# Optimization experiments

Hardware: AMD Instinct MI355X
Metric: run time of the kernel (lower is better)

## Reference

```python
import jax, jax.numpy as jnp
import numpy as np

VOCAB = 32000
EMBED = 512
UNITS = 64  # LSTM hidden size hardcoded in the source
B, T = 32, 128
T_ENC = 128


def setup_inputs() -> dict:
    key = jax.random.key(0)
    ks = jax.random.split(key, 10)
    decoder_inputs = jax.random.randint(ks[0], (B, T), 0, VOCAB)
    encoder_inputs = jax.random.normal(ks[1], (B, T_ENC, UNITS), jnp.float32)
    h0 = 0.1 * jax.random.normal(ks[2], (B, UNITS), jnp.float32)
    c0 = 0.1 * jax.random.normal(ks[3], (B, UNITS), jnp.float32)
    emb = 0.02 * jax.random.normal(ks[4], (VOCAB, EMBED), jnp.float32)
    Wx = 0.05 * jax.random.normal(ks[5], (EMBED, 4 * UNITS), jnp.float32)
    Wh = 0.05 * jax.random.normal(ks[6], (UNITS, 4 * UNITS), jnp.float32)
    # keras unit_forget_bias=True: forget-gate bias initialized to 1
    b = jnp.zeros((4 * UNITS,), jnp.float32).at[UNITS:2 * UNITS].set(1.0)
    Wd = 0.02 * jax.random.normal(ks[7], (2 * UNITS, VOCAB), jnp.float32)
    bd = jnp.zeros((VOCAB,), jnp.float32)
    return {"encoder_inputs": encoder_inputs, "decoder_inputs": decoder_inputs,
            "h0": h0, "c0": c0, "emb": emb, "Wx": Wx, "Wh": Wh, "b": b,
            "Wd": Wd, "bd": bd}


def reference(encoder_inputs, decoder_inputs, h0, c0, emb, Wx, Wh, b, Wd, bd):
    # Embedding (dropout layers are identity at inference)
    x = emb[decoder_inputs]                      # [B, T, E]
    # Precompute input contribution to all gates for all timesteps
    xz = jnp.einsum('bte,eg->btg', x, Wx) + b    # [B, T, 4U]

    def step(carry, zt):
        h, c = carry
        z = zt + h @ Wh                           # [B, 4U]
        i, f, g, o = jnp.split(z, 4, axis=-1)     # keras gate order i,f,c,o
        i = jax.nn.sigmoid(i)
        f = jax.nn.sigmoid(f)
        o = jax.nn.sigmoid(o)
        c_new = f * c + i * jnp.tanh(g)
        h_new = o * jnp.tanh(c_new)
        return (h_new, c_new), h_new

    (hT, cT), hs = jax.lax.scan(step, (h0, c0), jnp.swapaxes(xz, 0, 1))
    seq = jnp.swapaxes(hs, 0, 1)                  # [B, T, U]

    # key_value = concat(h0, seq[:, :-1])  -> queries for Luong attention
    kv = jnp.concatenate([h0[:, None, :], seq[:, :-1, :]], axis=1)  # [B, T, U]
    # keras Attention([q, v]): scores = q @ v^T, softmax, ctx = attn @ v
    scores = jnp.einsum('btu,bsu->bts', kv, encoder_inputs)         # [B, T, T_enc]
    attn = jax.nn.softmax(scores, axis=-1)
    ctx = jnp.einsum('bts,bsu->btu', attn, encoder_inputs)          # [B, T, U]

    feat = jnp.concatenate([seq, ctx], axis=-1)   # [B, T, 2U]
    out = jax.nn.softmax(jnp.einsum('btu,uv->btv', feat, Wd) + bd, axis=-1)
    return out, hT, cT
```

## Files before the change

### kernel.cpp

```cpp
#include <hip/hip_runtime.h>
#include <hip/hip_bf16.h>
#include <math.h>

#define B_   32
#define T_   128
#define TE_  128
#define U_   64
#define E_   512
#define V_   32000
#define G_   256

typedef __attribute__((ext_vector_type(8))) short  short8x;
typedef __attribute__((ext_vector_type(4))) float  f32x4;
typedef __attribute__((ext_vector_type(4))) unsigned short u16x4;

__device__ inline unsigned short f2bf(float x) {
    union { float f; unsigned int u; } v; v.f = x;
    unsigned int u = v.u;
    u = (u + 0x7FFFu + ((u >> 16) & 1u)) >> 16;
    return (unsigned short)u;
}

__global__ void embed_xz_kernel(const int* __restrict__ dec,
                                const float* __restrict__ emb,
                                const float* __restrict__ Wx,
                                const float* __restrict__ bias,
                                float* __restrict__ xz) {
    __shared__ float xs[16][E_];
    int tid = threadIdx.x;
    int rb = blockIdx.x * 16;
#pragma unroll
    for (int i = 0; i < 8; i++) {
        int idx = tid + i * 256;
        int r = idx >> 7, q = idx & 127;
        ((float4*)xs[r])[q] = ((const float4*)(emb + (size_t)dec[rb + r] * E_))[q];
    }
    __syncthreads();
    float acc[16];
#pragma unroll
    for (int r = 0; r < 16; r++) acc[r] = 0.f;
    for (int e = 0; e < E_; e += 4) {
        float w0 = Wx[(e + 0) * G_ + tid];
        float w1 = Wx[(e + 1) * G_ + tid];
        float w2 = Wx[(e + 2) * G_ + tid];
        float w3 = Wx[(e + 3) * G_ + tid];
#pragma unroll
        for (int r = 0; r < 16; r++) {
            float4 xv = *(const float4*)&xs[r][e];
            acc[r] += xv.x * w0 + xv.y * w1 + xv.z * w2 + xv.w * w3;
        }
    }
    float bv = bias[tid];
#pragma unroll
    for (int r = 0; r < 16; r++)
        xz[(size_t)(rb + r) * G_ + tid] = acc[r] + bv;
}

__global__ void lstm_kernel(const float* __restrict__ xz,
                            const float* __restrict__ h0,
                            const float* __restrict__ c0,
                            const float* __restrict__ Wh,
                            float* __restrict__ feat,
                            float* __restrict__ hT,
                            float* __restrict__ cT) {
    int b = blockIdx.x;
    int g = threadIdx.x;
    float w[U_];
#pragma unroll
    for (int u = 0; u < U_; u++) w[u] = Wh[u * G_ + g];
    __shared__ float h[U_];
    __shared__ float c[U_];
    __shared__ float z[G_];
    if (g < U_) { h[g] = h0[b * U_ + g]; c[g] = c0[b * U_ + g]; }
    __syncthreads();
    const float* xzb = xz + (size_t)b * T_ * G_;
    for (int t = 0; t < T_; t++) {
        float acc = xzb[t * G_ + g];
#pragma unroll
        for (int u4 = 0; u4 < U_ / 4; u4++) {
            float4 hv = *(const float4*)&h[u4 * 4];
            acc += hv.x * w[u4 * 4 + 0] + hv.y * w[u4 * 4 + 1] +
                   hv.z * w[u4 * 4 + 2] + hv.w * w[u4 * 4 + 3];
        }
        z[g] = acc;
        __syncthreads();
        if (g < U_) {
            float iv = 1.f / (1.f + expf(-z[g]));
            float fv = 1.f / (1.f + expf(-z[U_ + g]));
            float gv = tanhf(z[2 * U_ + g]);
            float ov = 1.f / (1.f + expf(-z[3 * U_ + g]));
            float cn = fv * c[g] + iv * gv;
            float hn = ov * tanhf(cn);
            c[g] = cn; h[g] = hn;
            feat[((size_t)b * T_ + t) * 2 * U_ + g] = hn;
        }
        __syncthreads();
    }
    if (g < U_) { hT[b * U_ + g] = h[g]; cT[b * U_ + g] = c[g]; }
}

__global__ void attn_kernel(const float* __restrict__ enc,
                            const float* __restrict__ h0,
                            float* __restrict__ feat) {
    int row = blockIdx.x;
    int b = row >> 7;
    int t = row & (T_ - 1);
    int tid = threadIdx.x;
    __shared__ float kv[U_];
    __shared__ float at[TE_];
    __shared__ float red[TE_];
    if (tid < U_)
        kv[tid] = (t == 0) ? h0[b * U_ + tid] : feat[(size_t)(row - 1) * 2 * U_ + tid];
    __syncthreads();
    const float* encb = enc + (size_t)b * TE_ * U_;
    float s = 0.f;
    const float4* e4 = (const float4*)(encb + tid * U_);
#pragma unroll
    for (int u4 = 0; u4 < U_ / 4; u4++) {
        float4 ev = e4[u4];
        s += ev.x * kv[u4 * 4 + 0] + ev.y * kv[u4 * 4 + 1] +
             ev.z * kv[u4 * 4 + 2] + ev.w * kv[u4 * 4 + 3];
    }
    red[tid] = s;
    __syncthreads();
    for (int off = 64; off > 0; off >>= 1) {
        if (tid < off) red[tid] = fmaxf(red[tid], red[tid + off]);
        __syncthreads();
    }
    float m = red[0];
    __syncthreads();
    float e = expf(s - m);
    at[tid] = e;
    red[tid] = e;
    __syncthreads();
    for (int off = 64; off > 0; off >>= 1) {
        if (tid < off) red[tid] += red[tid + off];
        __syncthreads();
    }
    float inv_sum = 1.f / red[0];
    __syncthreads();
    if (tid < U_) {
        float cacc = 0.f;
#pragma unroll 4
        for (int sx = 0; sx < TE_; sx++)
            cacc += at[sx] * encb[sx * U_ + tid];
        feat[(size_t)row * 2 * U_ + U_ + tid] = cacc * inv_sum;
    }
}

__global__ void feat_to_bf16(const float* __restrict__ feat,
                             unsigned short* __restrict__ fb) {
    int i = blockIdx.x * 256 + threadIdx.x;
    float4 v = ((const float4*)feat)[i];
    u16x4 o;
    o.x = f2bf(v.x); o.y = f2bf(v.y); o.z = f2bf(v.z); o.w = f2bf(v.w);
    *(u16x4*)(fb + (size_t)i * 4) = o;
}

__global__ void wd_transpose(const float* __restrict__ Wd,
                             unsigned short* __restrict__ wdt) {
    __shared__ float t[128][65];
    int tid = threadIdx.x;
    int nb = blockIdx.x * 64;
#pragma unroll
    for (int i = 0; i < 32; i++) {
        int idx = tid + i * 256;
        int k = idx >> 6, n = idx & 63;
        t[k][n] = Wd[(size_t)k * V_ + nb + n];
    }
    __syncthreads();
    int n = tid >> 2, kq = tid & 3;
#pragma unroll
    for (int g = 0; g < 4; g++) {
        short8x s;
#pragma unroll
        for (int j = 0; j < 8; j++)
            s[j] = (short)f2bf(t[kq * 32 + g * 8 + j][n]);
        *(short8x*)(wdt + (size_t)(nb + n) * 128 + kq * 32 + g * 8) = s;
    }
}

__device__ inline void gemm_block_map(int L, int& rowblk, int& colblk) {
    int W = (L & 7) * 200 + (L >> 3);
    colblk = W >> 6;
    rowblk = W & 63;
}

__global__ void gemm_stats(const unsigned short* __restrict__ fb,
                           const unsigned short* __restrict__ wdt,
                           const float* __restrict__ bd,
                           float* __restrict__ partial) {
    int rowblk, cb;
    gemm_block_map(blockIdx.x, rowblk, cb);
    int tid = threadIdx.x;
    int lane = tid & 63, wave = tid >> 6;
    int lrow = lane & 15, quad = lane >> 4;
    int rowbase = rowblk * 64 + wave * 16;
    int col0 = cb * 1280;

    short8x a[4];
    const unsigned short* ap = fb + (size_t)(rowbase + lrow) * 128 + quad * 8;
#pragma unroll
    for (int k = 0; k < 4; k++) a[k] = *(const short8x*)(ap + k * 32);

    float s[4] = {0.f, 0.f, 0.f, 0.f};
    for (int ch = 0; ch < 10; ch++) {
        int cc = col0 + ch * 128;
        f32x4 acc[8];
#pragma unroll
        for (int ct = 0; ct < 8; ct++) acc[ct] = {0.f, 0.f, 0.f, 0.f};
        const unsigned short* bp = wdt + (size_t)(cc + lrow) * 128 + quad * 8;
#pragma unroll
        for (int ct = 0; ct < 8; ct++) {
#pragma unroll
            for (int k = 0; k < 4; k++) {
                short8x b = *(const short8x*)(bp + (size_t)ct * 16 * 128 + k * 32);
                acc[ct] = __builtin_amdgcn_mfma_f32_16x16x32_bf16(a[k], b, acc[ct], 0, 0, 0);
            }
        }
#pragma unroll
        for (int ct = 0; ct < 8; ct++) {
            float bdv = bd[cc + ct * 16 + lrow];
#pragma unroll
            for (int r = 0; r < 4; r++)
                s[r] += __expf(acc[ct][r] + bdv);
        }
    }
#pragma unroll
    for (int r = 0; r < 4; r++) {
        float v = s[r];
        v += __shfl_xor(v, 1);
        v += __shfl_xor(v, 2);
        v += __shfl_xor(v, 4);
        v += __shfl_xor(v, 8);
        if (lrow == 0)
            partial[(size_t)(rowbase + quad * 4 + r) * 25 + cb] = v;
    }
}

__global__ void merge_stats(const float* __restrict__ partial,
                            float* __restrict__ inv_s) {
    int r = blockIdx.x * 256 + threadIdx.x;
    float s = 0.f;
#pragma unroll
    for (int i = 0; i < 25; i++) s += partial[(size_t)r * 25 + i];
    inv_s[r] = 1.f / s;
}

__global__ void gemm_norm(const unsigned short* __restrict__ fb,
                          const unsigned short* __restrict__ wdt,
                          const float* __restrict__ bd,
                          const float* __restrict__ inv_s,
                          float* __restrict__ out) {
    __shared__ float lds[64 * 132];
    int rowblkI, cbI;
    gemm_block_map(blockIdx.x, rowblkI, cbI);
    int tid = threadIdx.x;
    int lane = tid & 63, wave = tid >> 6;
    int lrow = lane & 15, quad = lane >> 4;
    int rowblk = rowblkI * 64;
    int rowbase = rowblk + wave * 16;
    int col0 = cbI * 1280;

    short8x a[4];
    const unsigned short* ap = fb + (size_t)(rowbase + lrow) * 128 + quad * 8;
#pragma unroll
    for (int k = 0; k < 4; k++) a[k] = *(const short8x*)(ap + k * 32);

    float inv[4];
#pragma unroll
    for (int r = 0; r < 4; r++) inv[r] = inv_s[rowbase + quad * 4 + r];

    for (int ch = 0; ch < 10; ch++) {
        int cc = col0 + ch * 128;
        f32x4 acc[8];
#pragma unroll
        for (int ct = 0; ct < 8; ct++) acc[ct] = {0.f, 0.f, 0.f, 0.f};
        const unsigned short* bp = wdt + (size_t)(cc + lrow) * 128 + quad * 8;
#pragma unroll
        for (int ct = 0; ct < 8; ct++) {
#pragma unroll
            for (int k = 0; k < 4; k++) {
                short8x b = *(const short8x*)(bp + (size_t)ct * 16 * 128 + k * 32);
                acc[ct] = __builtin_amdgcn_mfma_f32_16x16x32_bf16(a[k], b, acc[ct], 0, 0, 0);
            }
        }
        __syncthreads();
#pragma unroll
        for (int ct = 0; ct < 8; ct++) {
            float bdv = bd[cc + ct * 16 + lrow];
#pragma unroll
            for (int r = 0; r < 4; r++)
                lds[(wave * 16 + quad * 4 + r) * 132 + ct * 16 + lrow] =
                    __expf(acc[ct][r] + bdv) * inv[r];
        }
        __syncthreads();
#pragma unroll
        for (int i = 0; i < 8; i++) {
            int idx = tid + i * 256;
            int r = idx >> 5, c4 = idx & 31;
            f32x4 v = *(f32x4*)&lds[r * 132 + c4 * 4];
            __builtin_nontemporal_store(v,
                (f32x4*)(out + (size_t)(rowblk + r) * V_ + cc + c4 * 4));
        }
    }
}

extern "C" void kernel_launch(void* const* d_in, const int* in_sizes, int n_in,
                              void* d_out, int out_size, void* d_ws, size_t ws_size,
                              hipStream_t stream) {
    const float* enc  = (const float*)d_in[0];
    const int*   dec  = (const int*)d_in[1];
    const float* h0   = (const float*)d_in[2];
    const float* c0   = (const float*)d_in[3];
    const float* emb  = (const float*)d_in[4];
    const float* Wx   = (const float*)d_in[5];
    const float* Wh   = (const float*)d_in[6];
    const float* bias = (const float*)d_in[7];
    const float* Wd   = (const float*)d_in[8];
    const float* bd   = (const float*)d_in[9];
    float* out = (float*)d_out;
    float* ws  = (float*)d_ws;

    const int NROW = B_ * T_;
    float* xz      = ws;
    float* feat    = xz + (size_t)NROW * G_;
    float* partial = feat + (size_t)NROW * 2 * U_;
    float* inv_s   = partial + (size_t)NROW * 25;
    unsigned short* fb  = (unsigned short*)(inv_s + NROW);
    unsigned short* wdt = (unsigned short*)(fb + (size_t)NROW * 2 * U_);
    float* hT = out + (size_t)NROW * V_;
    float* cT = hT + B_ * U_;

    wd_transpose<<<dim3(V_ / 64), 256, 0, stream>>>(Wd, wdt);
    embed_xz_kernel<<<dim3(NROW / 16), 256, 0, stream>>>(dec, emb, Wx, bias, xz);
    lstm_kernel<<<dim3(B_), 256, 0, stream>>>(xz, h0, c0, Wh, feat, hT, cT);
    attn_kernel<<<dim3(NROW), 128, 0, stream>>>(enc, h0, feat);
    feat_to_bf16<<<dim3(NROW * 2 * U_ / 1024), 256, 0, stream>>>(feat, fb);
    gemm_stats<<<dim3(1600), 256, 0, stream>>>(fb, wdt, bd, partial);
    merge_stats<<<dim3(NROW / 256), 256, 0, stream>>>(partial, inv_s);
    gemm_norm<<<dim3(1600), 256, 0, stream>>>(fb, wdt, bd, inv_s, out);
}
```

Baseline: 1.222 ms.

## Double GEMM row tiles, fuse bf16 conversion, and prefetch xz in LSTM

Each wave in both vocab GEMM kernels now computes two 16-row tiles, so every B fragment loaded from wdt feeds two MFMAs. This halves the grid and the redundant weight traffic. The bf16 conversion kernel is removed: the LSTM and attention kernels write bf16 features directly. The LSTM loop also prefetches the next timestep's xz and splits the dot product into four independent accumulators to shorten the dependency chain. The costs are higher register pressure in the GEMMs and fewer blocks for occupancy.

```diff
diff --git a/kernel.cpp b/kernel.cpp
--- a/kernel.cpp
+++ b/kernel.cpp
@@ -61,6 +61,7 @@
                             const float* __restrict__ c0,
                             const float* __restrict__ Wh,
                             float* __restrict__ feat,
+                            unsigned short* __restrict__ fb,
                             float* __restrict__ hT,
                             float* __restrict__ cT) {
     int b = blockIdx.x;
@@ -72,17 +73,29 @@
     __shared__ float c[U_];
     __shared__ float z[G_];
     if (g < U_) { h[g] = h0[b * U_ + g]; c[g] = c0[b * U_ + g]; }
-    __syncthreads();
     const float* xzb = xz + (size_t)b * T_ * G_;
+    float xznext = xzb[g];
+    __syncthreads();
     for (int t = 0; t < T_; t++) {
-        float acc = xzb[t * G_ + g];
-#pragma unroll
-        for (int u4 = 0; u4 < U_ / 4; u4++) {
-            float4 hv = *(const float4*)&h[u4 * 4];
-            acc += hv.x * w[u4 * 4 + 0] + hv.y * w[u4 * 4 + 1] +
-                   hv.z * w[u4 * 4 + 2] + hv.w * w[u4 * 4 + 3];
-        }
-        z[g] = acc;
+        float ac0 = xznext, ac1 = 0.f, ac2 = 0.f, ac3 = 0.f;
+        int tn = (t + 1 < T_) ? t + 1 : t;
+        xznext = xzb[tn * G_ + g];
+#pragma unroll
+        for (int u4 = 0; u4 < 16; u4 += 4) {
+            float4 h0v = *(const float4*)&h[(u4 + 0) * 4];
+            float4 h1v = *(const float4*)&h[(u4 + 1) * 4];
+            float4 h2v = *(const float4*)&h[(u4 + 2) * 4];
+            float4 h3v = *(const float4*)&h[(u4 + 3) * 4];
+            ac0 += h0v.x * w[(u4+0)*4+0] + h0v.y * w[(u4+0)*4+1] +
+                   h0v.z * w[(u4+0)*4+2] + h0v.w * w[(u4+0)*4+3];
+            ac1 += h1v.x * w[(u4+1)*4+0] + h1v.y * w[(u4+1)*4+1] +
+                   h1v.z * w[(u4+1)*4+2] + h1v.w * w[(u4+1)*4+3];
+            ac2 += h2v.x * w[(u4+2)*4+0] + h2v.y * w[(u4+2)*4+1] +
+                   h2v.z * w[(u4+2)*4+2] + h2v.w * w[(u4+2)*4+3];
+            ac3 += h3v.x * w[(u4+3)*4+0] + h3v.y * w[(u4+3)*4+1] +
+                   h3v.z * w[(u4+3)*4+2] + h3v.w * w[(u4+3)*4+3];
+        }
+        z[g] = (ac0 + ac1) + (ac2 + ac3);
         __syncthreads();
         if (g < U_) {
             float iv = 1.f / (1.f + expf(-z[g]));
@@ -92,7 +105,9 @@
             float cn = fv * c[g] + iv * gv;
             float hn = ov * tanhf(cn);
             c[g] = cn; h[g] = hn;
-            feat[((size_t)b * T_ + t) * 2 * U_ + g] = hn;
+            size_t row = (size_t)b * T_ + t;
+            feat[row * 2 * U_ + g] = hn;
+            fb[row * 2 * U_ + g] = f2bf(hn);
         }
         __syncthreads();
     }
@@ -101,7 +116,8 @@
 
 __global__ void attn_kernel(const float* __restrict__ enc,
                             const float* __restrict__ h0,
-                            float* __restrict__ feat) {
+                            const float* __restrict__ feat,
+                            unsigned short* __restrict__ fb) {
     int row = blockIdx.x;
     int b = row >> 7;
     int t = row & (T_ - 1);
@@ -144,17 +160,8 @@
 #pragma unroll 4
         for (int sx = 0; sx < TE_; sx++)
             cacc += at[sx] * encb[sx * U_ + tid];
-        feat[(size_t)row * 2 * U_ + U_ + tid] = cacc * inv_sum;
-    }
-}
-
-__global__ void feat_to_bf16(const float* __restrict__ feat,
-                             unsigned short* __restrict__ fb) {
-    int i = blockIdx.x * 256 + threadIdx.x;
-    float4 v = ((const float4*)feat)[i];
-    u16x4 o;
-    o.x = f2bf(v.x); o.y = f2bf(v.y); o.z = f2bf(v.z); o.w = f2bf(v.w);
-    *(u16x4*)(fb + (size_t)i * 4) = o;
+        fb[(size_t)row * 2 * U_ + U_ + tid] = f2bf(cacc * inv_sum);
+    }
 }
 
 __global__ void wd_transpose(const float* __restrict__ Wd,
@@ -181,9 +188,9 @@
 }
 
 __device__ inline void gemm_block_map(int L, int& rowblk, int& colblk) {
-    int W = (L & 7) * 200 + (L >> 3);
-    colblk = W >> 6;
-    rowblk = W & 63;
+    int W = (L & 7) * 100 + (L >> 3);
+    colblk = W >> 5;
+    rowblk = W & 31;
 }
 
 __global__ void gemm_stats(const unsigned short* __restrict__ fb,
@@ -195,47 +202,57 @@
     int tid = threadIdx.x;
     int lane = tid & 63, wave = tid >> 6;
     int lrow = lane & 15, quad = lane >> 4;
-    int rowbase = rowblk * 64 + wave * 16;
+    int rowbase = rowblk * 128 + wave * 32;
     int col0 = cb * 1280;
 
-    short8x a[4];
-    const unsigned short* ap = fb + (size_t)(rowbase + lrow) * 128 + quad * 8;
-#pragma unroll
-    for (int k = 0; k < 4; k++) a[k] = *(const short8x*)(ap + k * 32);
-
-    float s[4] = {0.f, 0.f, 0.f, 0.f};
+    short8x a[2][4];
+#pragma unroll
+    for (int rt = 0; rt < 2; rt++) {
+        const unsigned short* ap = fb + (size_t)(rowbase + rt * 16 + lrow) * 128 + quad * 8;
+#pragma unroll
+        for (int k = 0; k < 4; k++) a[rt][k] = *(const short8x*)(ap + k * 32);
+    }
+
+    float s[2][4] = {{0.f,0.f,0.f,0.f},{0.f,0.f,0.f,0.f}};
     for (int ch = 0; ch < 10; ch++) {
         int cc = col0 + ch * 128;
-        f32x4 acc[8];
-#pragma unroll
-        for (int ct = 0; ct < 8; ct++) acc[ct] = {0.f, 0.f, 0.f, 0.f};
+        f32x4 acc[2][8];
+#pragma unroll
+        for (int rt = 0; rt < 2; rt++)
+#pragma unroll
+            for (int ct = 0; ct < 8; ct++) acc[rt][ct] = {0.f, 0.f, 0.f, 0.f};
         const unsigned short* bp = wdt + (size_t)(cc + lrow) * 128 + quad * 8;
 #pragma unroll
         for (int ct = 0; ct < 8; ct++) {
 #pragma unroll
             for (int k = 0; k < 4; k++) {
                 short8x b = *(const short8x*)(bp + (size_t)ct * 16 * 128 + k * 32);
-                acc[ct] = __builtin_amdgcn_mfma_f32_16x16x32_bf16(a[k], b, acc[ct], 0, 0, 0);
+                acc[0][ct] = __builtin_amdgcn_mfma_f32_16x16x32_bf16(a[0][k], b, acc[0][ct], 0, 0, 0);
+                acc[1][ct] = __builtin_amdgcn_mfma_f32_16x16x32_bf16(a[1][k], b, acc[1][ct], 0, 0, 0);
             }
         }
 #pragma unroll
         for (int ct = 0; ct < 8; ct++) {
             float bdv = bd[cc + ct * 16 + lrow];
 #pragma unroll
-            for (int r = 0; r < 4; r++)
-                s[r] += __expf(acc[ct][r] + bdv);
-        }
-    }
-#pragma unroll
-    for (int r = 0; r < 4; r++) {
-        float v = s[r];
-        v += __shfl_xor(v, 1);
-        v += __shfl_xor(v, 2);
-        v += __shfl_xor(v, 4);
-        v += __shfl_xor(v, 8);
-        if (lrow == 0)
-            partial[(size_t)(rowbase + quad * 4 + r) * 25 + cb] = v;
-    }
+            for (int rt = 0; rt < 2; rt++)
+#pragma unroll
+                for (int r = 0; r < 4; r++)
+                    s[rt][r] += __expf(acc[rt][ct][r] + bdv);
+        }
+    }
+#pragma unroll
+    for (int rt = 0; rt < 2; rt++)
+#pragma unroll
+        for (int r = 0; r < 4; r++) {
+            float v = s[rt][r];
+            v += __shfl_xor(v, 1);
+            v += __shfl_xor(v, 2);
+            v += __shfl_xor(v, 4);
+            v += __shfl_xor(v, 8);
+            if (lrow == 0)
+                partial[(size_t)(rowbase + rt * 16 + quad * 4 + r) * 25 + cb] = v;
+        }
 }
 
 __global__ void merge_stats(const float* __restrict__ partial,
@@ -258,50 +275,63 @@
     int tid = threadIdx.x;
     int lane = tid & 63, wave = tid >> 6;
     int lrow = lane & 15, quad = lane >> 4;
-    int rowblk = rowblkI * 64;
-    int rowbase = rowblk + wave * 16;
+    int rowblk = rowblkI * 128;
+    int rowbase = rowblk + wave * 32;
     int col0 = cbI * 1280;
 
-    short8x a[4];
-    const unsigned short* ap = fb + (size_t)(rowbase + lrow) * 128 + quad * 8;
-#pragma unroll
-    for (int k = 0; k < 4; k++) a[k] = *(const short8x*)(ap + k * 32);
-
-    float inv[4];
-#pragma unroll
-    for (int r = 0; r < 4; r++) inv[r] = inv_s[rowbase + quad * 4 + r];
+    short8x a[2][4];
+#pragma unroll
+    for (int rt = 0; rt < 2; rt++) {
+        const unsigned short* ap = fb + (size_t)(rowbase + rt * 16 + lrow) * 128 + quad * 8;
+#pragma unroll
+        for (int k = 0; k < 4; k++) a[rt][k] = *(const short8x*)(ap + k * 32);
+    }
+
+    float inv[2][4];
+#pragma unroll
+    for (int rt = 0; rt < 2; rt++)
+#pragma unroll
+        for (int r = 0; r < 4; r++)
+            inv[rt][r] = inv_s[rowbase + rt * 16 + quad * 4 + r];
 
     for (int ch = 0; ch < 10; ch++) {
         int cc = col0 + ch * 128;
-        f32x4 acc[8];
-#pragma unroll
-        for (int ct = 0; ct < 8; ct++) acc[ct] = {0.f, 0.f, 0.f, 0.f};
+        f32x4 acc[2][8];
+#pragma unroll
+        for (int rt = 0; rt < 2; rt++)
+#pragma unroll
+            for (int ct = 0; ct < 8; ct++) acc[rt][ct] = {0.f, 0.f, 0.f, 0.f};
         const unsigned short* bp = wdt + (size_t)(cc + lrow) * 128 + quad * 8;
 #pragma unroll
         for (int ct = 0; ct < 8; ct++) {
 #pragma unroll
             for (int k = 0; k < 4; k++) {
                 short8x b = *(const short8x*)(bp + (size_t)ct * 16 * 128 + k * 32);
-                acc[ct] = __builtin_amdgcn_mfma_f32_16x16x32_bf16(a[k], b, acc[ct], 0, 0, 0);
+                acc[0][ct] = __builtin_amdgcn_mfma_f32_16x16x32_bf16(a[0][k], b, acc[0][ct], 0, 0, 0);
+                acc[1][ct] = __builtin_amdgcn_mfma_f32_16x16x32_bf16(a[1][k], b, acc[1][ct], 0, 0, 0);
             }
         }
-        __syncthreads();
-#pragma unroll
-        for (int ct = 0; ct < 8; ct++) {
-            float bdv = bd[cc + ct * 16 + lrow];
-#pragma unroll
-            for (int r = 0; r < 4; r++)
-                lds[(wave * 16 + quad * 4 + r) * 132 + ct * 16 + lrow] =
-                    __expf(acc[ct][r] + bdv) * inv[r];
-        }
-        __syncthreads();
-#pragma unroll
-        for (int i = 0; i < 8; i++) {
-            int idx = tid + i * 256;
-            int r = idx >> 5, c4 = idx & 31;
-            f32x4 v = *(f32x4*)&lds[r * 132 + c4 * 4];
-            __builtin_nontemporal_store(v,
-                (f32x4*)(out + (size_t)(rowblk + r) * V_ + cc + c4 * 4));
+#pragma unroll
+        for (int rt = 0; rt < 2; rt++) {
+            __syncthreads();
+#pragma unroll
+            for (int ct = 0; ct < 8; ct++) {
+                float bdv = bd[cc + ct * 16 + lrow];
+#pragma unroll
+                for (int r = 0; r < 4; r++)
+                    lds[(wave * 16 + quad * 4 + r) * 132 + ct * 16 + lrow] =
+                        __expf(acc[rt][ct][r] + bdv) * inv[rt][r];
+            }
+            __syncthreads();
+#pragma unroll
+            for (int i = 0; i < 8; i++) {
+                int idx = tid + i * 256;
+                int l = idx >> 5, c4 = idx & 31;
+                int orow = rowblk + (l >> 4) * 32 + rt * 16 + (l & 15);
+                f32x4 v = *(f32x4*)&lds[l * 132 + c4 * 4];
+                __builtin_nontemporal_store(v,
+                    (f32x4*)(out + (size_t)orow * V_ + cc + c4 * 4));
+            }
         }
     }
 }
@@ -334,10 +364,9 @@
 
     wd_transpose<<<dim3(V_ / 64), 256, 0, stream>>>(Wd, wdt);
     embed_xz_kernel<<<dim3(NROW / 16), 256, 0, stream>>>(dec, emb, Wx, bias, xz);
-    lstm_kernel<<<dim3(B_), 256, 0, stream>>>(xz, h0, c0, Wh, feat, hT, cT);
-    attn_kernel<<<dim3(NROW), 128, 0, stream>>>(enc, h0, feat);
-    feat_to_bf16<<<dim3(NROW * 2 * U_ / 1024), 256, 0, stream>>>(feat, fb);
-    gemm_stats<<<dim3(1600), 256, 0, stream>>>(fb, wdt, bd, partial);
+    lstm_kernel<<<dim3(B_), 256, 0, stream>>>(xz, h0, c0, Wh, feat, fb, hT, cT);
+    attn_kernel<<<dim3(NROW), 128, 0, stream>>>(enc, h0, feat, fb);
+    gemm_stats<<<dim3(800), 256, 0, stream>>>(fb, wdt, bd, partial);
     merge_stats<<<dim3(NROW / 256), 256, 0, stream>>>(partial, inv_s);
-    gemm_norm<<<dim3(1600), 256, 0, stream>>>(fb, wdt, bd, inv_s, out);
-}
+    gemm_norm<<<dim3(800), 256, 0, stream>>>(fb, wdt, bd, inv_s, out);
+}
```

Result: faster. 1.060 ms (-13.3%).
